# Kernel tuning notes

Hardware: AMD Instinct MI355X
Metric: run time of the kernel (lower is better)

## Reference

```python
import jax, jax.numpy as jnp
import numpy as np

B, T, D = 2, 1024, 2048
H, HKV, DH = 16, 4, 128
G = H // HKV  # GQA groups
F = 5632
ROPE_THETA = 10000.0
EPS = 1e-6


def _rope_tables(t, dh, theta):
    inv = 1.0 / (theta ** (np.arange(0, dh, 2, dtype=np.float32) / dh))  # [dh//2]
    ang = np.outer(np.arange(t, dtype=np.float32), inv)                  # [T, dh//2]
    return jnp.asarray(np.cos(ang)), jnp.asarray(np.sin(ang))


def setup_inputs() -> dict:
    key = jax.random.key(0)
    ks = jax.random.split(key, 9)
    s = 0.02
    cos, sin = _rope_tables(T, DH, ROPE_THETA)
    return {
        "x": jax.random.normal(ks[0], (B, T, D), jnp.float32),
        "freqs_cos": cos,
        "freqs_sin": sin,
        "w_norm1": jnp.ones((D,), jnp.float32),
        "w_norm2": jnp.ones((D,), jnp.float32),
        "wq": jax.random.normal(ks[1], (D, H * DH), jnp.float32) * s,
        "wk": jax.random.normal(ks[2], (D, HKV * DH), jnp.float32) * s,
        "wv": jax.random.normal(ks[3], (D, HKV * DH), jnp.float32) * s,
        "wo": jax.random.normal(ks[4], (D, D), jnp.float32) * s,
        "w1": jax.random.normal(ks[5], (D, F), jnp.float32) * s,
        "w2": jax.random.normal(ks[6], (F, D), jnp.float32) * s,
        "w3": jax.random.normal(ks[7], (D, F), jnp.float32) * s,
    }


def _rmsnorm(x, w):
    var = jnp.mean(jnp.square(x), axis=-1, keepdims=True)
    return x * jax.lax.rsqrt(var + EPS) * w


def _apply_rope(x, cos, sin):
    # x: [B, T, nH, DH]; cos/sin: [T, DH//2]
    xr = x.reshape(*x.shape[:-1], DH // 2, 2)
    x0, x1 = xr[..., 0], xr[..., 1]
    c = cos[None, :, None, :]
    s = sin[None, :, None, :]
    o0 = x0 * c - x1 * s
    o1 = x0 * s + x1 * c
    return jnp.stack([o0, o1], axis=-1).reshape(x.shape)


def reference(x, freqs_cos, freqs_sin, w_norm1, w_norm2, wq, wk, wv, wo, w1, w2, w3):
    residual = x
    xn = _rmsnorm(x, w_norm1)
    q = (xn @ wq).reshape(B, T, H, DH)
    k = (xn @ wk).reshape(B, T, HKV, DH)
    v = (xn @ wv).reshape(B, T, HKV, DH)
    q = _apply_rope(q, freqs_cos, freqs_sin)
    k = _apply_rope(k, freqs_cos, freqs_sin)
    # grouped heads: q -> [B, HKV, G, T, DH]; k,v -> [B, HKV, T, DH]
    q = q.transpose(0, 2, 1, 3).reshape(B, HKV, G, T, DH)
    k = k.transpose(0, 2, 1, 3)
    v = v.transpose(0, 2, 1, 3)
    scale = DH ** -0.5
    scores = jnp.einsum("bkgtd,bksd->bkgts", q, k) * scale  # [B,HKV,G,T,T]
    causal = jnp.tril(jnp.ones((T, T), dtype=bool))
    scores = jnp.where(causal, scores, -jnp.inf)
    attn = jax.nn.softmax(scores, axis=-1)
    out = jnp.einsum("bkgts,bksd->bkgtd", attn, v)  # [B,HKV,G,T,DH]
    out = out.reshape(B, H, T, DH).transpose(0, 2, 1, 3).reshape(B, T, D)
    x = residual + out @ wo
    h = _rmsnorm(x, w_norm2)
    ffn = (jax.nn.silu(h @ w1) * (h @ w3)) @ w2
    return x + ffn
```

## Files before the change

### kernel.cpp

```cpp
#include <hip/hip_runtime.h>
#include <hip/hip_bf16.h>
#include <math.h>

typedef __hip_bfloat16 bf16;
typedef __attribute__((ext_vector_type(8))) short bf16x8;
typedef __attribute__((ext_vector_type(4))) float f32x4;

__device__ __forceinline__ float b2f(bf16 v) { return __bfloat162float(v); }
__device__ __forceinline__ bf16  f2b(float v) { return __float2bfloat16(v); }

constexpr int Bc = 2, Tc = 1024, Dc = 2048, Hc = 16, HKVc = 4, DHc = 128, Fc = 5632;
constexpr int Mr = Bc * Tc;
constexpr int Nqkv = Hc * DHc + 2 * HKVc * DHc;

__device__ __forceinline__ void g2l16(void* lds, const void* g) {
  __builtin_amdgcn_global_load_lds(
      (const __attribute__((address_space(1))) unsigned int*)g,
      (__attribute__((address_space(3))) unsigned int*)lds, 16, 0, 0);
}

__global__ __launch_bounds__(256) void tcast_k(const float* __restrict__ src,
                                               bf16* __restrict__ dst,
                                               int N, int K) {
  __shared__ bf16 tile[64][68];
  const int t = threadIdx.x;
  const int n0 = blockIdx.x * 64, k0 = blockIdx.y * 64;
#pragma unroll
  for (int it = 0; it < 4; ++it) {
    const int kl = it * 16 + (t >> 4);
    const int nl = (t & 15) * 4;
    float4 v = *reinterpret_cast<const float4*>(src + (size_t)(k0 + kl) * N + n0 + nl);
    tile[kl][nl]     = f2b(v.x);
    tile[kl][nl + 1] = f2b(v.y);
    tile[kl][nl + 2] = f2b(v.z);
    tile[kl][nl + 3] = f2b(v.w);
  }
  __syncthreads();
  union { uint4 u; bf16 h[8]; } o;
#pragma unroll
  for (int it = 0; it < 2; ++it) {
    const int nl = it * 32 + (t >> 3);
    const int kl = (t & 7) * 8;
#pragma unroll
    for (int j = 0; j < 8; ++j) o.h[j] = tile[kl + j][nl];
    *reinterpret_cast<uint4*>(dst + (size_t)(n0 + nl) * K + k0 + kl) = o.u;
  }
}

__global__ __launch_bounds__(256) void rmsnorm_k(const float* __restrict__ x,
                                                 const float* __restrict__ w,
                                                 bf16* __restrict__ out) {
  const size_t rbase = (size_t)blockIdx.x * Dc;
  float ss = 0.f;
  for (int i = threadIdx.x; i < Dc; i += 256) {
    float v = x[rbase + i];
    ss += v * v;
  }
#pragma unroll
  for (int off = 32; off > 0; off >>= 1) ss += __shfl_down(ss, off, 64);
  __shared__ float red[4];
  const int lane = threadIdx.x & 63, wid = threadIdx.x >> 6;
  if (lane == 0) red[wid] = ss;
  __syncthreads();
  const float scale = rsqrtf((red[0] + red[1] + red[2] + red[3]) / (float)Dc + 1e-6f);
  for (int i = threadIdx.x; i < Dc; i += 256)
    out[rbase + i] = f2b(x[rbase + i] * scale * w[i]);
}

template <bool ADDRES>
__global__ __launch_bounds__(256) void gemm128(const bf16* __restrict__ A,
                                               const bf16* __restrict__ Bt,
                                               const float* __restrict__ Res,
                                               void* __restrict__ Out,
                                               int N, int K) {
  __shared__ __align__(16) bf16 As[128 * 32];
  __shared__ __align__(16) bf16 Bs[128 * 32];
  const int t = threadIdx.x;
  const int bm = blockIdx.y * 128, bn = blockIdx.x * 128;
  const int lane = t & 63, wv = t >> 6;
  const int wm = (wv & 1) * 64, wn = (wv >> 1) * 64;
  const int sr = t >> 2, sc = (t & 3) * 8;
  const bf16* ga = A + (size_t)(bm + sr) * K + sc;
  const bf16* gb = Bt + (size_t)(bn + sr) * K + sc;
  bf16* lA0 = As + sr * 32 + sc;
  bf16* lA1 = As + (64 + sr) * 32 + sc;
  bf16* lB0 = Bs + sr * 32 + sc;
  bf16* lB1 = Bs + (64 + sr) * 32 + sc;
  const size_t rstep = (size_t)64 * K;
  f32x4 acc[4][4] = {};
  const int fr = lane & 15, fko = (lane >> 4) * 8;
  for (int k0 = 0; k0 < K; k0 += 32) {
    __syncthreads();
    g2l16(lA0, ga + k0);
    g2l16(lA1, ga + rstep + k0);
    g2l16(lB0, gb + k0);
    g2l16(lB1, gb + rstep + k0);
    __syncthreads();
    bf16x8 af[4], bff[4];
#pragma unroll
    for (int i = 0; i < 4; ++i)
      af[i] = *reinterpret_cast<const bf16x8*>(As + (wm + i * 16 + fr) * 32 + fko);
#pragma unroll
    for (int j = 0; j < 4; ++j)
      bff[j] = *reinterpret_cast<const bf16x8*>(Bs + (wn + j * 16 + fr) * 32 + fko);
#pragma unroll
    for (int i = 0; i < 4; ++i)
#pragma unroll
      for (int j = 0; j < 4; ++j)
        acc[i][j] = __builtin_amdgcn_mfma_f32_16x16x32_bf16(af[i], bff[j], acc[i][j], 0, 0, 0);
  }
  const int er = (lane >> 4) * 4, ec = lane & 15;
#pragma unroll
  for (int i = 0; i < 4; ++i)
#pragma unroll
    for (int j = 0; j < 4; ++j) {
      const int row = bm + wm + i * 16 + er;
      const int col = bn + wn + j * 16 + ec;
#pragma unroll
      for (int r = 0; r < 4; ++r) {
        const size_t idx = (size_t)(row + r) * N + col;
        if (ADDRES) ((float*)Out)[idx] = Res[idx] + acc[i][j][r];
        else        ((bf16*)Out)[idx] = f2b(acc[i][j][r]);
      }
    }
}

__global__ __launch_bounds__(256) void ffn_dual(const bf16* __restrict__ A,
                                                const bf16* __restrict__ W1t,
                                                const bf16* __restrict__ W3t,
                                                bf16* __restrict__ act,
                                                int K) {
  __shared__ __align__(16) bf16 As[128 * 32];
  __shared__ __align__(16) bf16 B1s[64 * 32];
  __shared__ __align__(16) bf16 B3s[64 * 32];
  const int t = threadIdx.x;
  const int bm = blockIdx.y * 128, bn = blockIdx.x * 64;
  const int lane = t & 63, wv = t >> 6;
  const int wm = (wv & 1) * 64, wn = (wv >> 1) * 32;
  const int sr = t >> 2, sc = (t & 3) * 8;
  const bf16* ga = A + (size_t)(bm + sr) * K + sc;
  const bf16* g1 = W1t + (size_t)(bn + sr) * K + sc;
  const bf16* g3 = W3t + (size_t)(bn + sr) * K + sc;
  bf16* lA0 = As + sr * 32 + sc;
  bf16* lA1 = As + (64 + sr) * 32 + sc;
  bf16* l1  = B1s + sr * 32 + sc;
  bf16* l3  = B3s + sr * 32 + sc;
  const size_t rstep = (size_t)64 * K;
  f32x4 acc1[4][2] = {}, acc3[4][2] = {};
  const int fr = lane & 15, fko = (lane >> 4) * 8;
  for (int k0 = 0; k0 < K; k0 += 32) {
    __syncthreads();
    g2l16(lA0, ga + k0);
    g2l16(lA1, ga + rstep + k0);
    g2l16(l1, g1 + k0);
    g2l16(l3, g3 + k0);
    __syncthreads();
    bf16x8 af[4], b1[2], b3[2];
#pragma unroll
    for (int i = 0; i < 4; ++i)
      af[i] = *reinterpret_cast<const bf16x8*>(As + (wm + i * 16 + fr) * 32 + fko);
#pragma unroll
    for (int j = 0; j < 2; ++j) {
      b1[j] = *reinterpret_cast<const bf16x8*>(B1s + (wn + j * 16 + fr) * 32 + fko);
      b3[j] = *reinterpret_cast<const bf16x8*>(B3s + (wn + j * 16 + fr) * 32 + fko);
    }
#pragma unroll
    for (int i = 0; i < 4; ++i)
#pragma unroll
      for (int j = 0; j < 2; ++j) {
        acc1[i][j] = __builtin_amdgcn_mfma_f32_16x16x32_bf16(af[i], b1[j], acc1[i][j], 0, 0, 0);
        acc3[i][j] = __builtin_amdgcn_mfma_f32_16x16x32_bf16(af[i], b3[j], acc3[i][j], 0, 0, 0);
      }
  }
  const int er = (lane >> 4) * 4, ec = lane & 15;
#pragma unroll
  for (int i = 0; i < 4; ++i)
#pragma unroll
    for (int j = 0; j < 2; ++j) {
      const int row = bm + wm + i * 16 + er;
      const int col = bn + wn + j * 16 + ec;
#pragma unroll
      for (int r = 0; r < 4; ++r) {
        const float g = acc1[i][j][r], u = acc3[i][j][r];
        const float sg = g / (1.f + __expf(-g));
        act[(size_t)(row + r) * Fc + col] = f2b(sg * u);
      }
    }
}

__global__ __launch_bounds__(256) void repack_k(const bf16* __restrict__ qkv,
                                                const float* __restrict__ cosb,
                                                const float* __restrict__ sinb,
                                                bf16* __restrict__ Qr,
                                                bf16* __restrict__ Kr,
                                                bf16* __restrict__ Vt) {
  const int bt = blockIdx.x;
  const int b = bt >> 10, tp = bt & (Tc - 1);
  const int t0 = threadIdx.x;
  const bf16* row = qkv + (size_t)bt * Nqkv;
#pragma unroll
  for (int k = 0; k < 4; ++k) {
    int p2 = k * 256 + t0;
    int hh = p2 >> 6, i = p2 & 63;
    float c = cosb[tp * 64 + i], sn = sinb[tp * 64 + i];
    float x0 = b2f(row[hh * 128 + 2 * i]), x1 = b2f(row[hh * 128 + 2 * i + 1]);
    bf16* dst = Qr + ((size_t)(b * Hc + hh) * Tc + tp) * DHc + 2 * i;
    dst[0] = f2b(x0 * c - x1 * sn);
    dst[1] = f2b(x0 * sn + x1 * c);
  }
  {
    int hh = t0 >> 6, i = t0 & 63;
    float c = cosb[tp * 64 + i], sn = sinb[tp * 64 + i];
    float x0 = b2f(row[2048 + hh * 128 + 2 * i]), x1 = b2f(row[2048 + hh * 128 + 2 * i + 1]);
    bf16* dst = Kr + ((size_t)(b * HKVc + hh) * Tc + tp) * DHc + 2 * i;
    dst[0] = f2b(x0 * c - x1 * sn);
    dst[1] = f2b(x0 * sn + x1 * c);
  }
#pragma unroll
  for (int k = 0; k < 2; ++k) {
    int e = k * 256 + t0;
    int kvh = e >> 7, dd = e & 127;
    Vt[((size_t)(b * HKVc + kvh) * DHc + dd) * Tc + tp] = row[2560 + e];
  }
}

__global__ __launch_bounds__(256) void fattn(const bf16* __restrict__ Qr,
                                             const bf16* __restrict__ Kr,
                                             const bf16* __restrict__ Vt,
                                             bf16* __restrict__ ao) {
  __shared__ __align__(16) bf16 Ks[64 * 136];
  __shared__ __align__(16) bf16 Vts[128 * 72];
  __shared__ __align__(16) bf16 Ps[4][16 * 72];
  const int idx = blockIdx.x;
  const int r = idx & 15;
  const int qt = (r & 1) ? (15 - (r >> 1)) : (r >> 1);
  const int h = (idx >> 4) & 15;
  const int b = idx >> 8;
  const int kv = h >> 2;
  const int t = threadIdx.x, lane = t & 63, wv = t >> 6;
  const int fr = lane & 15, quad = lane >> 4;

  const bf16* Qbase = Qr + ((size_t)(b * Hc + h) * Tc + qt * 64) * DHc;
  const bf16* Kbase = Kr + (size_t)(b * HKVc + kv) * Tc * DHc;
  const bf16* Vbase = Vt + (size_t)(b * HKVc + kv) * DHc * Tc;

  bf16x8 qf[4];
#pragma unroll
  for (int c = 0; c < 4; ++c)
    qf[c] = *reinterpret_cast<const bf16x8*>(Qbase + (size_t)(wv * 16 + fr) * DHc + c * 32 + quad * 8);

  float m[4], l[4];
  f32x4 o[8] = {};
#pragma unroll
  for (int r2 = 0; r2 < 4; ++r2) { m[r2] = -3.0e38f; l[r2] = 0.f; }

  for (int kt = 0; kt <= qt; ++kt) {
    __syncthreads();
    {
      const bf16* src = Kbase + (size_t)kt * 64 * DHc;
#pragma unroll
      for (int i2 = 0; i2 < 4; ++i2) {
        int flat = i2 * 256 + t;
        int row = flat >> 4, c16 = flat & 15;
        uint4 v = *reinterpret_cast<const uint4*>(src + (size_t)row * DHc + c16 * 8);
        *reinterpret_cast<uint4*>(&Ks[row * 136 + c16 * 8]) = v;
      }
#pragma unroll
      for (int i2 = 0; i2 < 4; ++i2) {
        int flat = i2 * 256 + t;
        int row = flat >> 3, c8 = flat & 7;
        uint4 v = *reinterpret_cast<const uint4*>(Vbase + (size_t)row * Tc + kt * 64 + c8 * 8);
        *reinterpret_cast<uint4*>(&Vts[row * 72 + c8 * 8]) = v;
      }
    }
    __syncthreads();
    f32x4 s[4];
#pragma unroll
    for (int cb = 0; cb < 4; ++cb) {
      f32x4 acc = {};
#pragma unroll
      for (int kc = 0; kc < 4; ++kc) {
        bf16x8 kf = *reinterpret_cast<const bf16x8*>(&Ks[(cb * 16 + fr) * 136 + kc * 32 + quad * 8]);
        acc = __builtin_amdgcn_mfma_f32_16x16x32_bf16(qf[kc], kf, acc, 0, 0, 0);
      }
      s[cb] = acc * 0.08838834764831845f;
    }
    if (kt == qt) {
#pragma unroll
      for (int cb = 0; cb < 4; ++cb)
#pragma unroll
        for (int r2 = 0; r2 < 4; ++r2) {
          int key = cb * 16 + fr;
          int qg = wv * 16 + quad * 4 + r2;
          if (key > qg) s[cb][r2] = -3.0e38f;
        }
    }
    float tm[4], ts[4];
#pragma unroll
    for (int r2 = 0; r2 < 4; ++r2)
      tm[r2] = fmaxf(fmaxf(s[0][r2], s[1][r2]), fmaxf(s[2][r2], s[3][r2]));
#pragma unroll
    for (int off = 1; off < 16; off <<= 1)
#pragma unroll
      for (int r2 = 0; r2 < 4; ++r2)
        tm[r2] = fmaxf(tm[r2], __shfl_xor(tm[r2], off, 64));
    float al[4];
#pragma unroll
    for (int r2 = 0; r2 < 4; ++r2) {
      float mn = fmaxf(m[r2], tm[r2]);
      al[r2] = __expf(m[r2] - mn);
      m[r2] = mn;
      ts[r2] = 0.f;
    }
#pragma unroll
    for (int cb = 0; cb < 4; ++cb)
#pragma unroll
      for (int r2 = 0; r2 < 4; ++r2) {
        float e = __expf(s[cb][r2] - m[r2]);
        s[cb][r2] = e;
        ts[r2] += e;
      }
#pragma unroll
    for (int off = 1; off < 16; off <<= 1)
#pragma unroll
      for (int r2 = 0; r2 < 4; ++r2)
        ts[r2] += __shfl_xor(ts[r2], off, 64);
#pragma unroll
    for (int r2 = 0; r2 < 4; ++r2) l[r2] = l[r2] * al[r2] + ts[r2];
#pragma unroll
    for (int db = 0; db < 8; ++db)
#pragma unroll
      for (int r2 = 0; r2 < 4; ++r2) o[db][r2] *= al[r2];
    bf16* pw = Ps[wv];
#pragma unroll
    for (int cb = 0; cb < 4; ++cb)
#pragma unroll
      for (int r2 = 0; r2 < 4; ++r2)
        pw[(quad * 4 + r2) * 72 + cb * 16 + fr] = f2b(s[cb][r2]);
    bf16x8 pa[2];
    pa[0] = *reinterpret_cast<const bf16x8*>(&pw[fr * 72 + quad * 8]);
    pa[1] = *reinterpret_cast<const bf16x8*>(&pw[fr * 72 + 32 + quad * 8]);
#pragma unroll
    for (int db = 0; db < 8; ++db) {
      bf16x8 v0 = *reinterpret_cast<const bf16x8*>(&Vts[(db * 16 + fr) * 72 + quad * 8]);
      bf16x8 v1 = *reinterpret_cast<const bf16x8*>(&Vts[(db * 16 + fr) * 72 + 32 + quad * 8]);
      o[db] = __builtin_amdgcn_mfma_f32_16x16x32_bf16(pa[0], v0, o[db], 0, 0, 0);
      o[db] = __builtin_amdgcn_mfma_f32_16x16x32_bf16(pa[1], v1, o[db], 0, 0, 0);
    }
  }
#pragma unroll
  for (int r2 = 0; r2 < 4; ++r2) {
    float inv = 1.f / l[r2];
    int qg = qt * 64 + wv * 16 + quad * 4 + r2;
    bf16* orow = ao + (size_t)(b * Tc + qg) * Dc + h * DHc;
#pragma unroll
    for (int db = 0; db < 8; ++db)
      orow[db * 16 + fr] = f2b(o[db][r2] * inv);
  }
}

extern "C" void kernel_launch(void* const* d_in, const int* in_sizes, int n_in,
                              void* d_out, int out_size, void* d_ws, size_t ws_size,
                              hipStream_t stream) {
  const float* x    = (const float*)d_in[0];
  const float* fcos = (const float*)d_in[1];
  const float* fsin = (const float*)d_in[2];
  const float* wn1  = (const float*)d_in[3];
  const float* wn2  = (const float*)d_in[4];
  const float* wq   = (const float*)d_in[5];
  const float* wk   = (const float*)d_in[6];
  const float* wv   = (const float*)d_in[7];
  const float* wo   = (const float*)d_in[8];
  const float* w1   = (const float*)d_in[9];
  const float* w2   = (const float*)d_in[10];
  const float* w3   = (const float*)d_in[11];

  char* p = (char*)d_ws;
  bf16* wqkv_t = (bf16*)p;                 p += (size_t)Nqkv * Dc * 2;
  bf16* qkv    = (bf16*)p;                 p += (size_t)Mr * Nqkv * 2;
  float* xat   = (float*)d_ws;
  bf16* wo_t = (bf16*)p;                   p += (size_t)Dc * Dc * 2;
  bf16* w1t  = (bf16*)p;                   p += (size_t)Fc * Dc * 2;
  bf16* w2t  = w1t;
  bf16* w3t  = (bf16*)p;                   p += (size_t)Fc * Dc * 2;
  bf16* xn   = (bf16*)p;                   p += (size_t)Mr * Dc * 2;
  bf16* ao   = (bf16*)p;                   p += (size_t)Mr * Dc * 2;
  bf16* act  = (bf16*)p;                   p += (size_t)Mr * Fc * 2;
  bf16* hb = xn;
  bf16* Qr = act;
  bf16* Kr = act + (size_t)Mr * Hc * DHc;
  bf16* Vtb = Kr + (size_t)Mr * HKVc * DHc;

  const dim3 blk(256);
  tcast_k<<<dim3(32, 32), blk, 0, stream>>>(wq, wqkv_t, 2048, 2048);
  tcast_k<<<dim3(8, 32), blk, 0, stream>>>(wk, wqkv_t + (size_t)2048 * 2048, 512, 2048);
  tcast_k<<<dim3(8, 32), blk, 0, stream>>>(wv, wqkv_t + (size_t)2560 * 2048, 512, 2048);
  tcast_k<<<dim3(32, 32), blk, 0, stream>>>(wo, wo_t, 2048, 2048);
  tcast_k<<<dim3(88, 32), blk, 0, stream>>>(w1, w1t, 5632, 2048);
  tcast_k<<<dim3(88, 32), blk, 0, stream>>>(w3, w3t, 5632, 2048);

  rmsnorm_k<<<Mr, blk, 0, stream>>>(x, wn1, xn);
  gemm128<false><<<dim3(Nqkv / 128, Mr / 128), blk, 0, stream>>>(xn, wqkv_t, nullptr, qkv, Nqkv, Dc);
  repack_k<<<Mr, blk, 0, stream>>>(qkv, fcos, fsin, Qr, Kr, Vtb);
  fattn<<<Bc * Hc * 16, blk, 0, stream>>>(Qr, Kr, Vtb, ao);
  gemm128<true><<<dim3(Dc / 128, Mr / 128), blk, 0, stream>>>(ao, wo_t, x, xat, Dc, Dc);
  rmsnorm_k<<<Mr, blk, 0, stream>>>(xat, wn2, hb);
  ffn_dual<<<dim3(Fc / 64, Mr / 128), blk, 0, stream>>>(hb, w1t, w3t, act, Dc);
  tcast_k<<<dim3(32, 88), blk, 0, stream>>>(w2, w2t, 2048, 5632);
  gemm128<true><<<dim3(Dc / 128, Mr / 128), blk, 0, stream>>>(act, w2t, xat, (float*)d_out, Dc, Fc);
}
```

Before: 649.7 us.

## Interleave W1/W3 weights and use pipelined 256x256 tile FFN GEMM

Transposes W1 and W3 into a single interleaved weight matrix, alternating 16-row groups, so one GEMM computes gate and up together. The dual FFN kernel becomes a 512-thread 256x256-tile kernel with a 64-wide K step and XOR-swizzled LDS. It double-buffers A and triple-buffers B, issuing global-to-LDS loads interleaved with the MFMA sub-steps and using setprio and fine-grained waitcnt. The intent is more data reuse per tile and latency hidden by overlapping loads with compute, at the cost of heavy LDS use (160KB) and complex hand-scheduled synchronisation.

```diff
diff --git a/kernel.cpp b/kernel.cpp
--- a/kernel.cpp
+++ b/kernel.cpp
@@ -44,6 +44,36 @@
 #pragma unroll
     for (int j = 0; j < 8; ++j) o.h[j] = tile[kl + j][nl];
     *reinterpret_cast<uint4*>(dst + (size_t)(n0 + nl) * K + k0 + kl) = o.u;
+  }
+}
+
+__global__ __launch_bounds__(256) void tcast_ffn(const float* __restrict__ src,
+                                                 bf16* __restrict__ dst,
+                                                 int off) {
+  __shared__ bf16 tile[64][68];
+  const int t = threadIdx.x;
+  const int n0 = blockIdx.x * 64, k0 = blockIdx.y * 64;
+#pragma unroll
+  for (int it = 0; it < 4; ++it) {
+    const int kl = it * 16 + (t >> 4);
+    const int nl = (t & 15) * 4;
+    float4 v = *reinterpret_cast<const float4*>(src + (size_t)(k0 + kl) * Fc + n0 + nl);
+    tile[kl][nl]     = f2b(v.x);
+    tile[kl][nl + 1] = f2b(v.y);
+    tile[kl][nl + 2] = f2b(v.z);
+    tile[kl][nl + 3] = f2b(v.w);
+  }
+  __syncthreads();
+  union { uint4 u; bf16 h[8]; } o;
+#pragma unroll
+  for (int it = 0; it < 2; ++it) {
+    const int nl = it * 32 + (t >> 3);
+    const int kl = (t & 7) * 8;
+#pragma unroll
+    for (int j = 0; j < 8; ++j) o.h[j] = tile[kl + j][nl];
+    const int n = n0 + nl;
+    const int r = ((n >> 4) << 5) + (n & 15) + off;
+    *reinterpret_cast<uint4*>(dst + (size_t)r * Dc + k0 + kl) = o.u;
   }
 }
 
@@ -125,67 +155,118 @@
     }
 }
 
-__global__ __launch_bounds__(256) void ffn_dual(const bf16* __restrict__ A,
-                                                const bf16* __restrict__ W1t,
-                                                const bf16* __restrict__ W3t,
-                                                bf16* __restrict__ act,
-                                                int K) {
-  __shared__ __align__(16) bf16 As[128 * 32];
-  __shared__ __align__(16) bf16 B1s[64 * 32];
-  __shared__ __align__(16) bf16 B3s[64 * 32];
-  const int t = threadIdx.x;
-  const int bm = blockIdx.y * 128, bn = blockIdx.x * 64;
-  const int lane = t & 63, wv = t >> 6;
-  const int wm = (wv & 1) * 64, wn = (wv >> 1) * 32;
-  const int sr = t >> 2, sc = (t & 3) * 8;
-  const bf16* ga = A + (size_t)(bm + sr) * K + sc;
-  const bf16* g1 = W1t + (size_t)(bn + sr) * K + sc;
-  const bf16* g3 = W3t + (size_t)(bn + sr) * K + sc;
-  bf16* lA0 = As + sr * 32 + sc;
-  bf16* lA1 = As + (64 + sr) * 32 + sc;
-  bf16* l1  = B1s + sr * 32 + sc;
-  bf16* l3  = B3s + sr * 32 + sc;
+template <int K>
+__global__ __launch_bounds__(512, 2) void ffn_gemm256(const bf16* __restrict__ A,
+                                                      const bf16* __restrict__ B,
+                                                      bf16* __restrict__ act) {
+  constexpr int NT = K / 64;
+  constexpr int NIT = NT / 2;
+  __shared__ bf16 As[2 * 256 * 64];
+  __shared__ bf16 Bs[3 * 256 * 64];
+  const int tid = threadIdx.x;
+  const int lane = tid & 63, wv = tid >> 6;
+  const int wr = wv >> 2, wc = wv & 3;
+  const int fr = lane & 15, quad = lane >> 4;
+  const int swz = fr & 7;
+  const int bm = blockIdx.y * 256;
+  const int bn = blockIdx.x * 256;
+  const int lrow = tid >> 3;
+  const int scol = ((tid & 7) ^ (lrow & 7)) * 8;
   const size_t rstep = (size_t)64 * K;
-  f32x4 acc1[4][2] = {}, acc3[4][2] = {};
-  const int fr = lane & 15, fko = (lane >> 4) * 8;
-  for (int k0 = 0; k0 < K; k0 += 32) {
-    __syncthreads();
-    g2l16(lA0, ga + k0);
-    g2l16(lA1, ga + rstep + k0);
-    g2l16(l1, g1 + k0);
-    g2l16(l3, g3 + k0);
-    __syncthreads();
-    bf16x8 af[4], b1[2], b3[2];
-#pragma unroll
-    for (int i = 0; i < 4; ++i)
-      af[i] = *reinterpret_cast<const bf16x8*>(As + (wm + i * 16 + fr) * 32 + fko);
-#pragma unroll
-    for (int j = 0; j < 2; ++j) {
-      b1[j] = *reinterpret_cast<const bf16x8*>(B1s + (wn + j * 16 + fr) * 32 + fko);
-      b3[j] = *reinterpret_cast<const bf16x8*>(B3s + (wn + j * 16 + fr) * 32 + fko);
-    }
-#pragma unroll
-    for (int i = 0; i < 4; ++i)
-#pragma unroll
-      for (int j = 0; j < 2; ++j) {
-        acc1[i][j] = __builtin_amdgcn_mfma_f32_16x16x32_bf16(af[i], b1[j], acc1[i][j], 0, 0, 0);
-        acc3[i][j] = __builtin_amdgcn_mfma_f32_16x16x32_bf16(af[i], b3[j], acc3[i][j], 0, 0, 0);
-      }
-  }
-  const int er = (lane >> 4) * 4, ec = lane & 15;
-#pragma unroll
-  for (int i = 0; i < 4; ++i)
-#pragma unroll
-    for (int j = 0; j < 2; ++j) {
-      const int row = bm + wm + i * 16 + er;
-      const int col = bn + wn + j * 16 + ec;
+
+  auto stageA = [&](int t, int half) {
+    const int buf = (t & 1) * 16384;
+    const bf16* g = A + (size_t)(bm + half * 128 + lrow) * K + t * 64 + scol;
+    bf16* d = As + buf + half * 8192 + (size_t)tid * 8;
+    g2l16(d, g);
+    g2l16(d + 4096, g + rstep);
+  };
+  auto stageB = [&](int t, int half, int buf) {
+    const bf16* g = B + (size_t)(bn + half * 128 + lrow) * K + t * 64 + scol;
+    bf16* d = Bs + buf * 16384 + half * 8192 + (size_t)tid * 8;
+    g2l16(d, g);
+    g2l16(d + 4096, g + rstep);
+  };
+
+  f32x4 acc[8][4] = {};
+  const int u0 = (quad ^ swz) * 8;
+
+  stageA(0, 0); stageA(0, 1);
+  stageB(0, 0, 0); stageB(0, 1, 0);
+  stageB(1, 0, 1); stageB(1, 1, 1);
+  asm volatile("s_waitcnt vmcnt(4)" ::: "memory");
+  __builtin_amdgcn_s_barrier();
+
+  int rb0 = 0, rb1 = 1, sb = 2;
+  for (int it = 0; it < NIT; ++it) {
+    const int t1 = 2 * it + 1;
+#pragma unroll
+    for (int j = 0; j < 8; ++j) {
+      const int bufT = (j < 4) ? 0 : 16384;
+      const int bufB = ((j < 4) ? rb0 : rb1) * 16384;
+      const int qr4 = ((j & 3) >> 1) * 4, qc2 = ((j & 3) & 1) * 2;
+      bf16x8 af[4][2], bv[2][2];
+      const bf16* Ab = As + bufT + (size_t)(wr * 128 + fr) * 64;
+      const bf16* Bb = Bs + bufB + (size_t)(wc * 64 + fr) * 64;
+#pragma unroll
+      for (int ii = 0; ii < 4; ++ii) {
+        af[ii][0] = *reinterpret_cast<const bf16x8*>(Ab + (qr4 + ii) * 1024 + u0);
+        af[ii][1] = *reinterpret_cast<const bf16x8*>(Ab + (qr4 + ii) * 1024 + (u0 ^ 32));
+      }
+#pragma unroll
+      for (int jj = 0; jj < 2; ++jj) {
+        bv[jj][0] = *reinterpret_cast<const bf16x8*>(Bb + (qc2 + jj) * 1024 + u0);
+        bv[jj][1] = *reinterpret_cast<const bf16x8*>(Bb + (qc2 + jj) * 1024 + (u0 ^ 32));
+      }
+      if (j == 0)      stageA(t1, 0);
+      else if (j == 1) stageA(t1, 1);
+      else if (j == 2) { if (2 * it + 2 < NT) stageB(2 * it + 2, 0, sb); }
+      else if (j == 3) { if (2 * it + 2 < NT) stageB(2 * it + 2, 1, sb); }
+      else if (j == 4) { if (2 * it + 2 < NT) stageA(2 * it + 2, 0); }
+      else if (j == 5) { if (2 * it + 2 < NT) stageA(2 * it + 2, 1); }
+      else if (j == 6) { if (2 * it + 3 < NT) stageB(2 * it + 3, 0, rb0); }
+      else             { if (2 * it + 3 < NT) stageB(2 * it + 3, 1, rb0); }
+      __builtin_amdgcn_s_barrier();
+      asm volatile("s_waitcnt lgkmcnt(0)" ::: "memory");
+      __builtin_amdgcn_sched_barrier(0);
+      __builtin_amdgcn_s_setprio(1);
+#pragma unroll
+      for (int ii = 0; ii < 4; ++ii)
+#pragma unroll
+        for (int jj = 0; jj < 2; ++jj) {
+          acc[qr4 + ii][qc2 + jj] = __builtin_amdgcn_mfma_f32_16x16x32_bf16(
+              af[ii][0], bv[jj][0], acc[qr4 + ii][qc2 + jj], 0, 0, 0);
+          acc[qr4 + ii][qc2 + jj] = __builtin_amdgcn_mfma_f32_16x16x32_bf16(
+              af[ii][1], bv[jj][1], acc[qr4 + ii][qc2 + jj], 0, 0, 0);
+        }
+      __builtin_amdgcn_s_setprio(0);
+      if (j == 3) {
+        if (2 * it + 2 < NT) asm volatile("s_waitcnt vmcnt(4)" ::: "memory");
+        else                 asm volatile("s_waitcnt vmcnt(0)" ::: "memory");
+      } else if (j == 7) {
+        if (2 * it + 3 < NT)      asm volatile("s_waitcnt vmcnt(4)" ::: "memory");
+        else if (2 * it + 2 < NT) asm volatile("s_waitcnt vmcnt(0)" ::: "memory");
+      }
+      __builtin_amdgcn_s_barrier();
+    }
+    const int nrb0 = sb; sb = rb1; rb1 = rb0; rb0 = nrb0;
+  }
+
+  const int er = quad * 4, ec = lane & 15;
+#pragma unroll
+  for (int i = 0; i < 8; ++i) {
+    const int row = bm + wr * 128 + i * 16 + er;
+#pragma unroll
+    for (int jp = 0; jp < 2; ++jp) {
+      const f32x4 g = acc[i][2 * jp], u = acc[i][2 * jp + 1];
+      const int f = blockIdx.x * 128 + wc * 32 + jp * 16 + ec;
 #pragma unroll
       for (int r = 0; r < 4; ++r) {
-        const float g = acc1[i][j][r], u = acc3[i][j][r];
-        const float sg = g / (1.f + __expf(-g));
-        act[(size_t)(row + r) * Fc + col] = f2b(sg * u);
-      }
-    }
+        const float sg = g[r] / (1.f + __expf(-g[r]));
+        act[(size_t)(row + r) * Fc + f] = f2b(sg * u[r]);
+      }
+    }
+  }
 }
 
 __global__ __launch_bounds__(256) void repack_k(const bf16* __restrict__ qkv,
@@ -380,9 +461,8 @@
   bf16* qkv    = (bf16*)p;                 p += (size_t)Mr * Nqkv * 2;
   float* xat   = (float*)d_ws;
   bf16* wo_t = (bf16*)p;                   p += (size_t)Dc * Dc * 2;
-  bf16* w1t  = (bf16*)p;                   p += (size_t)Fc * Dc * 2;
-  bf16* w2t  = w1t;
-  bf16* w3t  = (bf16*)p;                   p += (size_t)Fc * Dc * 2;
+  bf16* w13t = (bf16*)p;                   p += (size_t)2 * Fc * Dc * 2;
+  bf16* w2t  = w13t;
   bf16* xn   = (bf16*)p;                   p += (size_t)Mr * Dc * 2;
   bf16* ao   = (bf16*)p;                   p += (size_t)Mr * Dc * 2;
   bf16* act  = (bf16*)p;                   p += (size_t)Mr * Fc * 2;
@@ -396,8 +476,8 @@
   tcast_k<<<dim3(8, 32), blk, 0, stream>>>(wk, wqkv_t + (size_t)2048 * 2048, 512, 2048);
   tcast_k<<<dim3(8, 32), blk, 0, stream>>>(wv, wqkv_t + (size_t)2560 * 2048, 512, 2048);
   tcast_k<<<dim3(32, 32), blk, 0, stream>>>(wo, wo_t, 2048, 2048);
-  tcast_k<<<dim3(88, 32), blk, 0, stream>>>(w1, w1t, 5632, 2048);
-  tcast_k<<<dim3(88, 32), blk, 0, stream>>>(w3, w3t, 5632, 2048);
+  tcast_ffn<<<dim3(88, 32), blk, 0, stream>>>(w1, w13t, 0);
+  tcast_ffn<<<dim3(88, 32), blk, 0, stream>>>(w3, w13t, 16);
 
   rmsnorm_k<<<Mr, blk, 0, stream>>>(x, wn1, xn);
   gemm128<false><<<dim3(Nqkv / 128, Mr / 128), blk, 0, stream>>>(xn, wqkv_t, nullptr, qkv, Nqkv, Dc);
@@ -405,7 +485,7 @@
   fattn<<<Bc * Hc * 16, blk, 0, stream>>>(Qr, Kr, Vtb, ao);
   gemm128<true><<<dim3(Dc / 128, Mr / 128), blk, 0, stream>>>(ao, wo_t, x, xat, Dc, Dc);
   rmsnorm_k<<<Mr, blk, 0, stream>>>(xat, wn2, hb);
-  ffn_dual<<<dim3(Fc / 64, Mr / 128), blk, 0, stream>>>(hb, w1t, w3t, act, Dc);
+  ffn_gemm256<Dc><<<dim3(2 * Fc / 256, Mr / 256), dim3(512), 0, stream>>>(hb, w13t, act);
   tcast_k<<<dim3(32, 88), blk, 0, stream>>>(w2, w2t, 2048, 5632);
   gemm128<true><<<dim3(Dc / 128, Mr / 128), blk, 0, stream>>>(act, w2t, xat, (float*)d_out, Dc, Fc);
 }
```

Result: no change. 645.1 us (-0.7%).
